# Performance work log

Hardware: AMD Instinct MI355X
Metric: run time of the kernel (lower is better)

Reference implementation:

```python
import jax, jax.numpy as jnp
import numpy as np

B, LQ, LK, D, H = 2, 1024, 1024, 1024, 16
DH = D // H


def setup_inputs() -> dict:
    key = jax.random.key(0)
    ks = jax.random.split(key, 14)
    s = 1.0 / np.sqrt(D)
    inp = {
        "q": jax.random.normal(ks[0], (B, LQ, D), jnp.float32),
        "k": jax.random.normal(ks[1], (B, LK, D), jnp.float32),
        "v": jax.random.normal(ks[2], (B, LK, D), jnp.float32),
        "Wq": jax.random.normal(ks[3], (D, D), jnp.float32) * s,
        "bq": jnp.zeros((D,), jnp.float32),
        "Wk": jax.random.normal(ks[4], (D, D), jnp.float32) * s,
        "bk": jnp.zeros((D,), jnp.float32),
        "Wv": jax.random.normal(ks[5], (D, D), jnp.float32) * s,
        "bv": jnp.zeros((D,), jnp.float32),
        "Wo": jax.random.normal(ks[6], (D, D), jnp.float32) * s,
        "bo": jnp.zeros((D,), jnp.float32),
        "logits_bias": jax.random.normal(ks[7], (B, LQ, LK), jnp.float32),
        "key_padding_mask": jax.random.randint(ks[8], (B, LK), 0, 2) > 0,
    }
    return inp


def _split_heads(x):
    b, l, _ = x.shape
    return x.reshape(b, l, H, DH).transpose(0, 2, 1, 3)  # [B,H,L,DH]


def reference(q, k, v, Wq, bq, Wk, bk, Wv, bv, Wo, bo, logits_bias, key_padding_mask):
    qh = _split_heads(q @ Wq.T + bq)  # [B,H,Lq,DH]
    kh = _split_heads(k @ Wk.T + bk)  # [B,H,Lk,DH]
    vh = _split_heads(v @ Wv.T + bv)  # [B,H,Lk,DH]

    neg = jnp.finfo(qh.dtype).min
    # attn_mask = logits_bias broadcast over heads, masked_fill at padded keys
    attn_mask = jnp.where(key_padding_mask[:, None, None, :],
                          neg, logits_bias[:, None, :, :])  # [B,1,Lq,Lk]

    scale = 1.0 / np.sqrt(DH)
    scores = jnp.einsum('bhqd,bhkd->bhqk', qh, kh) * scale + attn_mask
    probs = jax.nn.softmax(scores, axis=-1)
    out = jnp.einsum('bhqk,bhkd->bhqd', probs, vh)  # [B,H,Lq,DH]
    out = out.transpose(0, 2, 1, 3).reshape(q.shape[0], q.shape[1], D)
    return out @ Wo.T + bo
```

## Files before the change

### kernel.cpp

```cpp
#include <hip/hip_runtime.h>


typedef _Float16 half8 __attribute__((ext_vector_type(8)));
typedef _Float16 half4_t __attribute__((ext_vector_type(4)));
typedef __fp16 fp16x2 __attribute__((ext_vector_type(2)));
typedef float f32x4 __attribute__((ext_vector_type(4)));
typedef unsigned int u32;

#define MFMA16(a, b, c) __builtin_amdgcn_mfma_f32_16x16x32_f16((a), (b), (c), 0, 0, 0)

#define WAITCNT_VM(n) asm volatile("s_waitcnt vmcnt(" #n ")" ::: "memory")
#define WAITCNT_LGKM0() asm volatile("s_waitcnt lgkmcnt(0)" ::: "memory")
#define RAW_BARRIER() asm volatile("s_barrier" ::: "memory")
#define EXP2F(x) __builtin_amdgcn_exp2f(x)

__device__ __forceinline__ void gload16(const void* g, void* l) {
  __builtin_amdgcn_global_load_lds(
      (const __attribute__((address_space(1))) unsigned int*)g,
      (__attribute__((address_space(3))) unsigned int*)l, 16, 0, 0);
}

__device__ __forceinline__ half8 frag_ld(const _Float16* t, int row, int ck) {
  return *(const half8*)(t + row * 64 + (((ck ^ (row & 7)) << 3)));
}

__global__ __launch_bounds__(256) void cvt_f32_f16(
    const float* __restrict__ q, const float* __restrict__ k, const float* __restrict__ v,
    const float* __restrict__ Wq, const float* __restrict__ Wk,
    const float* __restrict__ Wv, const float* __restrict__ Wo,
    const float* __restrict__ biasL, const int* __restrict__ kpm,
    _Float16* __restrict__ q16, _Float16* __restrict__ k16, _Float16* __restrict__ v16,
    _Float16* __restrict__ w16, _Float16* __restrict__ biasC) {
  const int y = blockIdx.y;
  if (y == 5) {
    const size_t i = ((size_t)blockIdx.x * 256 + threadIdx.x) * 8;
    const int b = (int)(i >> 20);
    const int kk = (int)(i & 1023);
    const int* mrow = kpm + (b << 10) + kk;
    const float4 b0 = *(const float4*)(biasL + i);
    const float4 b1 = *(const float4*)(biasL + i + 4);
    const int4 m0 = *(const int4*)mrow;
    const int4 m1 = *(const int4*)(mrow + 4);
    const float sc = 1.44269504f;
    half8 h;
    h[0] = m0.x ? (_Float16)-30000.f : (_Float16)(b0.x * sc - 8.f);
    h[1] = m0.y ? (_Float16)-30000.f : (_Float16)(b0.y * sc - 8.f);
    h[2] = m0.z ? (_Float16)-30000.f : (_Float16)(b0.z * sc - 8.f);
    h[3] = m0.w ? (_Float16)-30000.f : (_Float16)(b0.w * sc - 8.f);
    h[4] = m1.x ? (_Float16)-30000.f : (_Float16)(b1.x * sc - 8.f);
    h[5] = m1.y ? (_Float16)-30000.f : (_Float16)(b1.y * sc - 8.f);
    h[6] = m1.z ? (_Float16)-30000.f : (_Float16)(b1.z * sc - 8.f);
    h[7] = m1.w ? (_Float16)-30000.f : (_Float16)(b1.w * sc - 8.f);
    *(half8*)(biasC + i) = h;
    return;
  }
  const float* s;
  _Float16* d;
  const size_t M = (size_t)1024 * 1024;
  int x = blockIdx.x;
  switch (y) {
    case 0: s = q;  d = q16; break;
    case 1: s = k;  d = k16; break;
    case 2: s = v;  d = v16; break;
    case 3: if (x < 512) { s = Wq; d = w16; } else { s = Wk; d = w16 + M; x -= 512; } break;
    default: if (x < 512) { s = Wv; d = w16 + 2 * M; } else { s = Wo; d = w16 + 3 * M; x -= 512; } break;
  }
  const size_t i = ((size_t)x * 256 + threadIdx.x) * 8;
  const float4 a = *(const float4*)(s + i);
  const float4 bvv = *(const float4*)(s + i + 4);
  half8 h;
  h[0] = (_Float16)a.x; h[1] = (_Float16)a.y; h[2] = (_Float16)a.z; h[3] = (_Float16)a.w;
  h[4] = (_Float16)bvv.x; h[5] = (_Float16)bvv.y; h[6] = (_Float16)bvv.z; h[7] = (_Float16)bvv.w;
  *(half8*)(d + i) = h;
}

__global__ __launch_bounds__(256, 2) void mmp_big(
    const _Float16* __restrict__ Aq, const _Float16* __restrict__ Ak,
    const _Float16* __restrict__ Av, const _Float16* __restrict__ W16,
    const float* __restrict__ c0, const float* __restrict__ c1,
    const float* __restrict__ c2, _Float16* __restrict__ Dq,
    _Float16* __restrict__ Dk, _Float16* __restrict__ Dvt) {
  __shared__ __align__(16) _Float16 lds[32768];

  const int tid = threadIdx.x;
  const int wv = tid >> 6, ln = tid & 63;
  const int quad = ln >> 4, col = ln & 15;
  const int wm = wv >> 1, wn = wv & 1;
  const int n0 = blockIdx.x * 128;
  const int m0 = blockIdx.y * 128;
  const int z = blockIdx.z;
  const bool swapped = (z < 2);

  const _Float16* A = (z == 0) ? Aq : (z == 1) ? Ak : Av;
  const _Float16* Bw = W16 + (size_t)z * 1024 * 1024;
  const float* bias = (z == 0) ? c0 : (z == 1) ? c1 : c2;

  auto stage = [&](int buf, int k0) {
#pragma unroll
    for (int j = 0; j < 8; ++j) {
      const int ci = j * 256 + tid;
      const _Float16* src;
      if (ci < 1024) {
        const int row = ci >> 3, lc = (ci & 7) ^ (row & 7);
        src = A + (size_t)(m0 + row) * 1024 + k0 + lc * 8;
      } else {
        const int di = ci - 1024;
        const int row = di >> 3, lc = (di & 7) ^ (row & 7);
        src = Bw + (size_t)(n0 + row) * 1024 + k0 + lc * 8;
      }
      gload16(src, lds + buf * 16384 + (j * 256 + wv * 64) * 8);
    }
  };

  const f32x4 zero4 = {0.f, 0.f, 0.f, 0.f};
  f32x4 acc[4][4];
#pragma unroll
  for (int i = 0; i < 4; ++i)
#pragma unroll
    for (int j = 0; j < 4; ++j) acc[i][j] = zero4;

  auto kstep = [&](const _Float16* As, const _Float16* Bs) {
    half8 af0[4], bf0[4], af1[4], bf1[4];
#pragma unroll
    for (int mi = 0; mi < 4; ++mi) af0[mi] = frag_ld(As, wm * 64 + mi * 16 + col, quad);
#pragma unroll
    for (int ni = 0; ni < 4; ++ni) bf0[ni] = frag_ld(Bs, wn * 64 + ni * 16 + col, quad);
#pragma unroll
    for (int mi = 0; mi < 4; ++mi) af1[mi] = frag_ld(As, wm * 64 + mi * 16 + col, 4 + quad);
#pragma unroll
    for (int ni = 0; ni < 4; ++ni) bf1[ni] = frag_ld(Bs, wn * 64 + ni * 16 + col, 4 + quad);
    WAITCNT_LGKM0();
    RAW_BARRIER();
    if (swapped) {
#pragma unroll
      for (int ni = 0; ni < 4; ++ni)
#pragma unroll
        for (int mi = 0; mi < 4; ++mi)
          acc[ni][mi] = MFMA16(bf0[ni], af0[mi], acc[ni][mi]);
#pragma unroll
      for (int ni = 0; ni < 4; ++ni)
#pragma unroll
        for (int mi = 0; mi < 4; ++mi)
          acc[ni][mi] = MFMA16(bf1[ni], af1[mi], acc[ni][mi]);
    } else {
#pragma unroll
      for (int mi = 0; mi < 4; ++mi)
#pragma unroll
        for (int ni = 0; ni < 4; ++ni)
          acc[mi][ni] = MFMA16(af0[mi], bf0[ni], acc[mi][ni]);
#pragma unroll
      for (int mi = 0; mi < 4; ++mi)
#pragma unroll
        for (int ni = 0; ni < 4; ++ni)
          acc[mi][ni] = MFMA16(af1[mi], bf1[ni], acc[mi][ni]);
    }
  };

  stage(0, 0);
  for (int i = 0; i < 15; ++i) {
    stage((i + 1) & 1, (i + 1) * 64);
    WAITCNT_VM(8);
    RAW_BARRIER();
    kstep(lds + (i & 1) * 16384, lds + (i & 1) * 16384 + 8192);
  }
  WAITCNT_VM(0);
  RAW_BARRIER();
  kstep(lds + 16384, lds + 16384 + 8192);

  if (swapped) {
    float4 bv4[4];
#pragma unroll
    for (int ni = 0; ni < 4; ++ni)
      bv4[ni] = *(const float4*)&bias[n0 + wn * 64 + ni * 16 + quad * 4];
    _Float16* D = z ? Dk : Dq;
#pragma unroll
    for (int ni = 0; ni < 4; ++ni) {
      const int n_g = n0 + wn * 64 + ni * 16 + quad * 4;
      const int h = n_g >> 6, dh = n_g & 63;
#pragma unroll
      for (int mi = 0; mi < 4; ++mi) {
        const int m_g = m0 + wm * 64 + mi * 16 + col;
        const int b = m_g >> 10, l = m_g & 1023;
        half4_t st;
        st[0] = (_Float16)(acc[ni][mi][0] + bv4[ni].x);
        st[1] = (_Float16)(acc[ni][mi][1] + bv4[ni].y);
        st[2] = (_Float16)(acc[ni][mi][2] + bv4[ni].z);
        st[3] = (_Float16)(acc[ni][mi][3] + bv4[ni].w);
        *(half4_t*)&D[((size_t)((b * 16 + h) * 1024) + l) * 64 + dh] = st;
      }
    }
  } else {
    float bv[4];
#pragma unroll
    for (int ni = 0; ni < 4; ++ni) bv[ni] = bias[n0 + wn * 64 + ni * 16 + col];
    __syncthreads();
    _Float16* Ct = lds;
#pragma unroll
    for (int mi = 0; mi < 4; ++mi) {
      const int ml = wm * 64 + mi * 16 + quad * 4;
#pragma unroll
      for (int ni = 0; ni < 4; ++ni) {
        const int nl = wn * 64 + ni * 16 + col;
        half4_t h;
#pragma unroll
        for (int r = 0; r < 4; ++r) h[r] = (_Float16)(acc[mi][ni][r] + bv[ni]);
        *(half4_t*)(Ct + (size_t)nl * 136 + ml) = h;
      }
    }
    __syncthreads();
#pragma unroll
    for (int it = 0; it < 8; ++it) {
      const int ci = it * 256 + tid;
      const int n = ci >> 4;
      const int mc = (ci & 15) * 8;
      const half8 hv = *(const half8*)(Ct + (size_t)n * 136 + mc);
      const int n_g = n0 + n;
      const int h = n_g >> 6, dh = n_g & 63;
      const int m_g = m0 + mc;
      const int b = m_g >> 10, l = m_g & 1023;
      *(half8*)(Dvt + ((size_t)((b * 16 + h) * 64 + dh)) * 1024 + l) = hv;
    }
  }
}

__global__ __launch_bounds__(256) void mmp_final(
    const _Float16* __restrict__ A, const _Float16* __restrict__ Bw,
    const float* __restrict__ bias, float* __restrict__ Df) {
  __shared__ __align__(16) _Float16 lds[24576];

  const int tid = threadIdx.x;
  const int wv = tid >> 6, ln = tid & 63;
  const int quad = ln >> 4, col = ln & 15;
  const int wm = wv >> 1, wn = wv & 1;
  const int n0 = blockIdx.x * 128;
  const int m0 = blockIdx.y * 64;

  auto stage = [&](int buf, int k0) {
#pragma unroll
    for (int j = 0; j < 6; ++j) {
      const int ci = j * 256 + tid;
      const _Float16* src;
      if (ci < 512) {
        const int row = ci >> 3, lc = (ci & 7) ^ (row & 7);
        src = A + (size_t)(m0 + row) * 1024 + k0 + lc * 8;
      } else {
        const int di = ci - 512;
        const int row = di >> 3, lc = (di & 7) ^ (row & 7);
        src = Bw + (size_t)(n0 + row) * 1024 + k0 + lc * 8;
      }
      gload16(src, lds + buf * 12288 + (j * 256 + wv * 64) * 8);
    }
  };

  const f32x4 zero4 = {0.f, 0.f, 0.f, 0.f};
  f32x4 acc[4][2];
#pragma unroll
  for (int i = 0; i < 4; ++i)
#pragma unroll
    for (int j = 0; j < 2; ++j) acc[i][j] = zero4;

  auto kstep = [&](const _Float16* As, const _Float16* Bs) {
    half8 af[2][2], bf[2][4];
#pragma unroll
    for (int kk = 0; kk < 2; ++kk) {
#pragma unroll
      for (int mi = 0; mi < 2; ++mi)
        af[kk][mi] = frag_ld(As, wm * 32 + mi * 16 + col, kk * 4 + quad);
#pragma unroll
      for (int ni = 0; ni < 4; ++ni)
        bf[kk][ni] = frag_ld(Bs, wn * 64 + ni * 16 + col, kk * 4 + quad);
    }
    WAITCNT_LGKM0();
    RAW_BARRIER();
#pragma unroll
    for (int kk = 0; kk < 2; ++kk)
#pragma unroll
      for (int ni = 0; ni < 4; ++ni)
#pragma unroll
        for (int mi = 0; mi < 2; ++mi)
          acc[ni][mi] = MFMA16(bf[kk][ni], af[kk][mi], acc[ni][mi]);
  };

  stage(0, 0);
  for (int i = 0; i < 15; ++i) {
    stage((i + 1) & 1, (i + 1) * 64);
    WAITCNT_VM(6);
    RAW_BARRIER();
    kstep(lds + (i & 1) * 12288, lds + (i & 1) * 12288 + 4096);
  }
  WAITCNT_VM(0);
  RAW_BARRIER();
  kstep(lds + 12288, lds + 12288 + 4096);

  float4 bv4[4];
#pragma unroll
  for (int ni = 0; ni < 4; ++ni)
    bv4[ni] = *(const float4*)&bias[n0 + wn * 64 + ni * 16 + quad * 4];
#pragma unroll
  for (int ni = 0; ni < 4; ++ni) {
    const int n_g = n0 + wn * 64 + ni * 16 + quad * 4;
#pragma unroll
    for (int mi = 0; mi < 2; ++mi) {
      const int m_g = m0 + wm * 32 + mi * 16 + col;
      float4 st;
      st.x = acc[ni][mi][0] + bv4[ni].x;
      st.y = acc[ni][mi][1] + bv4[ni].y;
      st.z = acc[ni][mi][2] + bv4[ni].z;
      st.w = acc[ni][mi][3] + bv4[ni].w;
      *(float4*)&Df[(size_t)m_g * 1024 + n_g] = st;
    }
  }
}

__global__ __launch_bounds__(512, 4) void attn(
    const _Float16* __restrict__ Qh, const _Float16* __restrict__ Kh,
    const _Float16* __restrict__ Vt, const _Float16* __restrict__ biasC,
    _Float16* __restrict__ AO) {
  __shared__ __align__(16) _Float16 KV[3 * 8192];

  const int tid = threadIdx.x;
  const int wv = tid >> 6, ln = tid & 63;
  const int quad = ln >> 4, col = ln & 15;
  const int qsub = wv >> 1, khalf = wv & 1;
  const int fid = blockIdx.x;
  const int xcd = fid & 7, g = fid >> 3;
  const int bh = (xcd << 2) | (g >> 4);
  const int q0 = (g & 15) * 64;
  const int b = bh >> 4, hh = bh & 15;
  const int qg = q0 + qsub * 16 + col;

  const _Float16* Qp = Qh + ((size_t)bh * 1024 + qg) * 64;
  const half8 bq0 = *(const half8*)(Qp + quad * 8);
  const half8 bq1 = *(const half8*)(Qp + 32 + quad * 8);
  WAITCNT_VM(0);

  const _Float16* biasRow = biasC + ((size_t)(b * 1024 + qg)) * 1024;

  auto stageKV = [&](int buf, int it) {
    const int koff = it * 64;
#pragma unroll
    for (int j = 0; j < 2; ++j) {
      const int ci = j * 512 + tid;
      const void* src;
      if (ci < 512) {
        const int row = ci >> 3, lc = (ci & 7) ^ (row & 7);
        src = Kh + ((size_t)bh * 1024 + koff + row) * 64 + lc * 8;
      } else {
        const int di = ci - 512;
        const int row = di >> 3, lc = (di & 7) ^ (row & 7);
        src = Vt + ((size_t)bh * 64 + row) * 1024 + koff + lc * 8;
      }
      gload16(src, KV + buf * 8192 + (j * 512 + wv * 64) * 8);
    }
  };
  auto loadBias = [&](int it, half4_t* bb) {
    const int koff = it * 64 + khalf * 32;
#pragma unroll
    for (int mi = 0; mi < 2; ++mi)
      bb[mi] = *(const half4_t*)&biasRow[koff + mi * 16 + quad * 4];
  };

  const f32x4 zero4 = {0.f, 0.f, 0.f, 0.f};
  f32x4 o[4];
#pragma unroll
  for (int ni = 0; ni < 4; ++ni) o[ni] = zero4;
  float l_i = 0.f;

  auto pk = [](float a, float bb) -> u32 {
    union { fp16x2 h; u32 u; } cv;
    cv.h = __builtin_amdgcn_cvt_pkrtz(a, bb);
    return cv.u;
  };

  auto compute = [&](int buf, const half4_t* bb) {
    const _Float16* Ks = KV + buf * 8192;
    const _Float16* Vs = Ks + 4096;
    f32x4 s[2];
#pragma unroll
    for (int mi = 0; mi < 2; ++mi) {
      f32x4 a4 = zero4;
      a4 = MFMA16(frag_ld(Ks, khalf * 32 + mi * 16 + col, quad), bq0, a4);
      a4 = MFMA16(frag_ld(Ks, khalf * 32 + mi * 16 + col, 4 + quad), bq1, a4);
      s[mi] = a4;
    }
#pragma unroll
    for (int mi = 0; mi < 2; ++mi)
#pragma unroll
      for (int r = 0; r < 4; ++r) {
        const float p = EXP2F(s[mi][r] * 0.18033688f + (float)bb[mi][r]);
        s[mi][r] = p;
        l_i += p;
      }
    const u32 X0 = pk(s[0][0], s[0][1]), X1 = pk(s[0][2], s[0][3]);
    const u32 Y0 = pk(s[1][0], s[1][1]), Y1 = pk(s[1][2], s[1][3]);
    const u32 tX0 = __shfl_xor(X0, 16), tX1 = __shfl_xor(X1, 16);
    const u32 tY0 = __shfl_xor(Y0, 16), tY1 = __shfl_xor(Y1, 16);
    const bool e = (quad & 1) == 0;
    const u32 L0 = e ? X0 : tX0, L1 = e ? X1 : tX1, L2 = e ? tX0 : X0, L3 = e ? tX1 : X1;
    const u32 H0 = e ? Y0 : tY0, H1 = e ? Y1 : tY1, H2 = e ? tY0 : Y0, H3 = e ? tY1 : Y1;
    const bool lo2 = quad < 2;
    const u32 W0 = lo2 ? H0 : L0, W1 = lo2 ? H1 : L1, W2 = lo2 ? H2 : L2, W3 = lo2 ? H3 : L3;
    const u32 R0 = __shfl_xor(W0, 32), R1 = __shfl_xor(W1, 32);
    const u32 R2 = __shfl_xor(W2, 32), R3 = __shfl_xor(W3, 32);
    const bool mid = (quad == 1) || (quad == 2);
    union { u32 u[4]; half8 h; } pf;
    pf.u[0] = mid ? R0 : (lo2 ? L0 : H0);
    pf.u[1] = mid ? R1 : (lo2 ? L1 : H1);
    pf.u[2] = mid ? R2 : (lo2 ? L2 : H2);
    pf.u[3] = mid ? R3 : (lo2 ? L3 : H3);
#pragma unroll
    for (int ni = 0; ni < 4; ++ni)
      o[ni] = MFMA16(frag_ld(Vs, ni * 16 + col, khalf * 4 + quad), pf.h, o[ni]);
  };

  half4_t bbA[2], bbB[2];
  stageKV(0, 0);
  loadBias(0, bbA);
#pragma unroll 3
  for (int i = 0; i < 15; ++i) {
    stageKV((i + 1) % 3, i + 1);
    loadBias(i + 1, bbB);
    WAITCNT_VM(4);
    WAITCNT_LGKM0();
    RAW_BARRIER();
    compute(i % 3, bbA);
    bbA[0] = bbB[0]; bbA[1] = bbB[1];
  }
  WAITCNT_VM(0);
  WAITCNT_LGKM0();
  RAW_BARRIER();
  compute(0, bbA);

  l_i += __shfl_xor(l_i, 16);
  l_i += __shfl_xor(l_i, 32);

  __syncthreads();
  f32x4* Ox = (f32x4*)&KV[0];
  float* MlS = (float*)&KV[8192];
  if (khalf == 1) {
#pragma unroll
    for (int ni = 0; ni < 4; ++ni) Ox[(qsub * 4 + ni) * 64 + ln] = o[ni];
    MlS[qsub * 64 + ln] = l_i;
  }
  __syncthreads();
  if (khalf == 0) {
    const float l2 = MlS[qsub * 64 + ln];
    const float inv = 1.0f / (l_i + l2);
#pragma unroll
    for (int ni = 0; ni < 4; ++ni) {
      const f32x4 o2 = Ox[(qsub * 4 + ni) * 64 + ln];
      half4_t h;
#pragma unroll
      for (int r = 0; r < 4; ++r)
        h[r] = (_Float16)((o[ni][r] + o2[r]) * inv);
      *(half4_t*)&AO[((size_t)(b * 1024 + qg)) * 1024 + hh * 64 + ni * 16 + quad * 4] = h;
    }
  }
}

extern "C" void kernel_launch(void* const* d_in, const int* in_sizes, int n_in,
                              void* d_out, int out_size, void* d_ws, size_t ws_size,
                              hipStream_t stream) {
  (void)in_sizes; (void)n_in; (void)out_size; (void)ws_size;
  const float* q = (const float*)d_in[0];
  const float* k = (const float*)d_in[1];
  const float* v = (const float*)d_in[2];
  const float* Wq = (const float*)d_in[3];
  const float* bq = (const float*)d_in[4];
  const float* Wk = (const float*)d_in[5];
  const float* bk = (const float*)d_in[6];
  const float* Wv = (const float*)d_in[7];
  const float* bv = (const float*)d_in[8];
  const float* Wo = (const float*)d_in[9];
  const float* bo = (const float*)d_in[10];
  const float* lb = (const float*)d_in[11];
  const int* kpm = (const int*)d_in[12];
  float* out = (float*)d_out;

  const size_t NT = (size_t)2 * 1024 * 1024;
  _Float16* q16 = (_Float16*)d_ws;
  _Float16* k16 = q16 + NT;
  _Float16* v16 = k16 + NT;
  _Float16* Qh = v16 + NT;
  _Float16* Kh = Qh + NT;
  _Float16* Vt = Kh + NT;
  _Float16* w16 = Vt + NT;
  _Float16* biasC = w16 + 4 * (NT / 2);
  _Float16* AO = q16;

  cvt_f32_f16<<<dim3(1024, 6), 256, 0, stream>>>(q, k, v, Wq, Wk, Wv, Wo, lb, kpm,
                                                 q16, k16, v16, w16, biasC);
  mmp_big<<<dim3(8, 16, 3), 256, 0, stream>>>(q16, k16, v16, w16, bq, bk, bv,
                                              Qh, Kh, Vt);
  attn<<<dim3(512), 512, 0, stream>>>(Qh, Kh, Vt, biasC, AO);
  mmp_final<<<dim3(8, 32), 256, 0, stream>>>(AO, w16 + 3 * NT / 2, bo, out);
}
```

Before: 169.4 us.

## Fuse bias/mask preprocessing into attention and remap GEMM blocks per XCD

Removes the separate bias/mask fp16 precompute pass from the conversion kernel and instead has the attention kernel read fp32 logits bias and the int key-padding mask directly, applying the scale and mask inline (masked keys give zero probability). This avoids writing and re-reading an intermediate fp16 bias tensor, but each attention block now reads fp32 bias twice as wide plus the mask per tile, 16 times over heads. Separately, both projection GEMMs use a flattened 1D grid with an XCD-aware block mapping so tiles that share operands land on the same XCD's L2.

```diff
diff --git a/kernel.cpp b/kernel.cpp
--- a/kernel.cpp
+++ b/kernel.cpp
@@ -28,32 +28,9 @@
     const float* __restrict__ q, const float* __restrict__ k, const float* __restrict__ v,
     const float* __restrict__ Wq, const float* __restrict__ Wk,
     const float* __restrict__ Wv, const float* __restrict__ Wo,
-    const float* __restrict__ biasL, const int* __restrict__ kpm,
     _Float16* __restrict__ q16, _Float16* __restrict__ k16, _Float16* __restrict__ v16,
-    _Float16* __restrict__ w16, _Float16* __restrict__ biasC) {
+    _Float16* __restrict__ w16) {
   const int y = blockIdx.y;
-  if (y == 5) {
-    const size_t i = ((size_t)blockIdx.x * 256 + threadIdx.x) * 8;
-    const int b = (int)(i >> 20);
-    const int kk = (int)(i & 1023);
-    const int* mrow = kpm + (b << 10) + kk;
-    const float4 b0 = *(const float4*)(biasL + i);
-    const float4 b1 = *(const float4*)(biasL + i + 4);
-    const int4 m0 = *(const int4*)mrow;
-    const int4 m1 = *(const int4*)(mrow + 4);
-    const float sc = 1.44269504f;
-    half8 h;
-    h[0] = m0.x ? (_Float16)-30000.f : (_Float16)(b0.x * sc - 8.f);
-    h[1] = m0.y ? (_Float16)-30000.f : (_Float16)(b0.y * sc - 8.f);
-    h[2] = m0.z ? (_Float16)-30000.f : (_Float16)(b0.z * sc - 8.f);
-    h[3] = m0.w ? (_Float16)-30000.f : (_Float16)(b0.w * sc - 8.f);
-    h[4] = m1.x ? (_Float16)-30000.f : (_Float16)(b1.x * sc - 8.f);
-    h[5] = m1.y ? (_Float16)-30000.f : (_Float16)(b1.y * sc - 8.f);
-    h[6] = m1.z ? (_Float16)-30000.f : (_Float16)(b1.z * sc - 8.f);
-    h[7] = m1.w ? (_Float16)-30000.f : (_Float16)(b1.w * sc - 8.f);
-    *(half8*)(biasC + i) = h;
-    return;
-  }
   const float* s;
   _Float16* d;
   const size_t M = (size_t)1024 * 1024;
@@ -86,9 +63,12 @@
   const int wv = tid >> 6, ln = tid & 63;
   const int quad = ln >> 4, col = ln & 15;
   const int wm = wv >> 1, wn = wv & 1;
-  const int n0 = blockIdx.x * 128;
-  const int m0 = blockIdx.y * 128;
-  const int z = blockIdx.z;
+  const int id = blockIdx.x;
+  const int xcd = id & 7, idx = id >> 3;
+  const int z = idx % 3;
+  const int sub = idx / 3;
+  const int n0 = ((xcd & 3) * 2 + (sub & 1)) * 128;
+  const int m0 = ((xcd >> 2) * 8 + (sub >> 1)) * 128;
   const bool swapped = (z < 2);
 
   const _Float16* A = (z == 0) ? Aq : (z == 1) ? Ak : Av;
@@ -232,8 +212,10 @@
   const int wv = tid >> 6, ln = tid & 63;
   const int quad = ln >> 4, col = ln & 15;
   const int wm = wv >> 1, wn = wv & 1;
-  const int n0 = blockIdx.x * 128;
-  const int m0 = blockIdx.y * 64;
+  const int id = blockIdx.x;
+  const int xcd = id & 7, idx = id >> 3;
+  const int n0 = ((xcd & 1) * 4 + (idx & 3)) * 128;
+  const int m0 = ((xcd >> 1) * 8 + (idx >> 2)) * 64;
 
   auto stage = [&](int buf, int k0) {
 #pragma unroll
@@ -314,8 +296,8 @@
 
 __global__ __launch_bounds__(512, 4) void attn(
     const _Float16* __restrict__ Qh, const _Float16* __restrict__ Kh,
-    const _Float16* __restrict__ Vt, const _Float16* __restrict__ biasC,
-    _Float16* __restrict__ AO) {
+    const _Float16* __restrict__ Vt, const float* __restrict__ biasL,
+    const int* __restrict__ kpm, _Float16* __restrict__ AO) {
   __shared__ __align__(16) _Float16 KV[3 * 8192];
 
   const int tid = threadIdx.x;
@@ -334,7 +316,8 @@
   const half8 bq1 = *(const half8*)(Qp + 32 + quad * 8);
   WAITCNT_VM(0);
 
-  const _Float16* biasRow = biasC + ((size_t)(b * 1024 + qg)) * 1024;
+  const float* biasRow = biasL + ((size_t)(b * 1024 + qg)) * 1024;
+  const int* kpmRow = kpm + b * 1024;
 
   auto stageKV = [&](int buf, int it) {
     const int koff = it * 64;
@@ -353,11 +336,14 @@
       gload16(src, KV + buf * 8192 + (j * 512 + wv * 64) * 8);
     }
   };
-  auto loadBias = [&](int it, half4_t* bb) {
+  auto loadBias = [&](int it, f32x4* bb, int4* mk) {
     const int koff = it * 64 + khalf * 32;
 #pragma unroll
-    for (int mi = 0; mi < 2; ++mi)
-      bb[mi] = *(const half4_t*)&biasRow[koff + mi * 16 + quad * 4];
+    for (int mi = 0; mi < 2; ++mi) {
+      const int kg = koff + mi * 16 + quad * 4;
+      bb[mi] = *(const f32x4*)&biasRow[kg];
+      mk[mi] = *(const int4*)&kpmRow[kg];
+    }
   };
 
   const f32x4 zero4 = {0.f, 0.f, 0.f, 0.f};
@@ -372,7 +358,7 @@
     return cv.u;
   };
 
-  auto compute = [&](int buf, const half4_t* bb) {
+  auto compute = [&](int buf, const f32x4* bb, const int4* mk) {
     const _Float16* Ks = KV + buf * 8192;
     const _Float16* Vs = Ks + 4096;
     f32x4 s[2];
@@ -384,13 +370,16 @@
       s[mi] = a4;
     }
 #pragma unroll
-    for (int mi = 0; mi < 2; ++mi)
+    for (int mi = 0; mi < 2; ++mi) {
+      const int* mp = (const int*)&mk[mi];
 #pragma unroll
       for (int r = 0; r < 4; ++r) {
-        const float p = EXP2F(s[mi][r] * 0.18033688f + (float)bb[mi][r]);
+        const float sv = s[mi][r] * 0.18033688f + (bb[mi][r] * 1.44269504f - 8.f);
+        const float p = mp[r] ? 0.f : EXP2F(sv);
         s[mi][r] = p;
         l_i += p;
       }
+    }
     const u32 X0 = pk(s[0][0], s[0][1]), X1 = pk(s[0][2], s[0][3]);
     const u32 Y0 = pk(s[1][0], s[1][1]), Y1 = pk(s[1][2], s[1][3]);
     const u32 tX0 = __shfl_xor(X0, 16), tX1 = __shfl_xor(X1, 16);
@@ -413,23 +402,25 @@
       o[ni] = MFMA16(frag_ld(Vs, ni * 16 + col, khalf * 4 + quad), pf.h, o[ni]);
   };
 
-  half4_t bbA[2], bbB[2];
+  f32x4 bbA[2], bbB[2];
+  int4 mkA[2], mkB[2];
   stageKV(0, 0);
-  loadBias(0, bbA);
+  loadBias(0, bbA, mkA);
 #pragma unroll 3
   for (int i = 0; i < 15; ++i) {
     stageKV((i + 1) % 3, i + 1);
-    loadBias(i + 1, bbB);
-    WAITCNT_VM(4);
+    loadBias(i + 1, bbB, mkB);
+    WAITCNT_VM(6);
     WAITCNT_LGKM0();
     RAW_BARRIER();
-    compute(i % 3, bbA);
+    compute(i % 3, bbA, mkA);
     bbA[0] = bbB[0]; bbA[1] = bbB[1];
+    mkA[0] = mkB[0]; mkA[1] = mkB[1];
   }
   WAITCNT_VM(0);
   WAITCNT_LGKM0();
   RAW_BARRIER();
-  compute(0, bbA);
+  compute(0, bbA, mkA);
 
   l_i += __shfl_xor(l_i, 16);
   l_i += __shfl_xor(l_i, 32);
@@ -485,13 +476,12 @@
   _Float16* Kh = Qh + NT;
   _Float16* Vt = Kh + NT;
   _Float16* w16 = Vt + NT;
-  _Float16* biasC = w16 + 4 * (NT / 2);
   _Float16* AO = q16;
 
-  cvt_f32_f16<<<dim3(1024, 6), 256, 0, stream>>>(q, k, v, Wq, Wk, Wv, Wo, lb, kpm,
-                                                 q16, k16, v16, w16, biasC);
-  mmp_big<<<dim3(8, 16, 3), 256, 0, stream>>>(q16, k16, v16, w16, bq, bk, bv,
-                                              Qh, Kh, Vt);
-  attn<<<dim3(512), 512, 0, stream>>>(Qh, Kh, Vt, biasC, AO);
-  mmp_final<<<dim3(8, 32), 256, 0, stream>>>(AO, w16 + 3 * NT / 2, bo, out);
-}
+  cvt_f32_f16<<<dim3(1024, 5), 256, 0, stream>>>(q, k, v, Wq, Wk, Wv, Wo,
+                                                 q16, k16, v16, w16);
+  mmp_big<<<dim3(384), 256, 0, stream>>>(q16, k16, v16, w16, bq, bk, bv,
+                                         Qh, Kh, Vt);
+  attn<<<dim3(512), 512, 0, stream>>>(Qh, Kh, Vt, lb, kpm, AO);
+  mmp_final<<<dim3(256), 256, 0, stream>>>(AO, w16 + 3 * NT / 2, bo, out);
+}
```

Measured after the change: 168.0 us (median of 2 runs). About the same (-0.8%).
